# Kernel optimization log

Hardware: AMD Instinct MI355X
Metric: run time of the kernel (lower is better)

The kernel has to match this reference:

```python
import jax, jax.numpy as jnp
import numpy as np

INDIM, HID, OUTDIM, T = 28, 128, 10, 28

def setup_inputs() -> dict:
    key = jax.random.key(0)
    ks = jax.random.split(key, 7)
    B = 65536
    bound1 = 1.0 / np.sqrt(INDIM)
    bound2 = 1.0 / np.sqrt(2 * HID)
    bound3 = 1.0 / np.sqrt(HID)
    return {
        "x": jax.random.normal(ks[0], (B, 784), dtype=jnp.float32),
        "W1": jax.random.uniform(ks[1], (INDIM, HID), jnp.float32, -bound1, bound1),
        "b1": jax.random.uniform(ks[2], (HID,), jnp.float32, -bound1, bound1),
        "W2": jax.random.uniform(ks[3], (2 * HID, HID), jnp.float32, -bound2, bound2),
        "b2": jax.random.uniform(ks[4], (HID,), jnp.float32, -bound2, bound2),
        "W3": jax.random.uniform(ks[5], (HID, OUTDIM), jnp.float32, -bound3, bound3),
        "b3": jax.random.uniform(ks[6], (OUTDIM,), jnp.float32, -bound3, bound3),
    }

def reference(x, W1, b1, W2, b2, W3, b3):
    B = x.shape[0]
    # (B, 784) -> (T, B, 28): scan over the 28 rows of each image
    rows = jnp.transpose(x.reshape(B, T, INDIM), (1, 0, 2))
    # W2 split: first HID rows multiply linear1 output, last HID rows multiply hidden state
    W2a, W2b = W2[:HID], W2[HID:]

    def step(h, row):
        t = row @ W1 + b1                      # (B, HID)
        h_new = jax.nn.relu(t @ W2a + h @ W2b + b2)  # concat(t, h) @ W2 == t@W2a + h@W2b
        return h_new, None

    h0 = jnp.zeros((B, HID), dtype=x.dtype)
    h_final, _ = jax.lax.scan(step, h0, rows)
    return h_final @ W3 + b3
```

## Files before the change

kernel.cpp:

```cpp
#include <hip/hip_runtime.h>

#define BTOT 65536
#define TST  28
#define PACK_DW 100
#define WXL_OFF 12800

typedef __attribute__((ext_vector_type(8))) short bf16x8;
typedef __attribute__((ext_vector_type(4))) float f32x4;
typedef __attribute__((ext_vector_type(2))) unsigned int u32x2;

__device__ __forceinline__ unsigned int f2bf(float f) {
    unsigned u = __float_as_uint(f);
    u += 0x7fff + ((u >> 16) & 1);
    return u >> 16;
}
__device__ __forceinline__ unsigned int pk2bf(float a, float b) {
    return f2bf(a) | (f2bf(b) << 16);
}
__device__ __forceinline__ bf16x8 cvt8(f32x4 a, f32x4 b) {
    union { unsigned int u[4]; bf16x8 v; } r;
    asm("v_cvt_pk_bf16_f32 %0, %1, %2" : "=v"(r.u[0]) : "v"(a[0]), "v"(a[1]));
    asm("v_cvt_pk_bf16_f32 %0, %1, %2" : "=v"(r.u[1]) : "v"(a[2]), "v"(a[3]));
    asm("v_cvt_pk_bf16_f32 %0, %1, %2" : "=v"(r.u[2]) : "v"(b[0]), "v"(b[1]));
    asm("v_cvt_pk_bf16_f32 %0, %1, %2" : "=v"(r.u[3]) : "v"(b[2]), "v"(b[3]));
    return r.v;
}

__global__ void pack1(const float* __restrict__ W1, const float* __restrict__ b1,
                      const float* __restrict__ W2, const float* __restrict__ b2,
                      const float* __restrict__ W3, const float* __restrict__ b3,
                      unsigned int* __restrict__ ws) {
    float* WxL = (float*)(ws + WXL_OFF);
    const int bid = blockIdx.x, tid = threadIdx.x;
    if (bid < 29) {
        const int k = bid, n = tid;
        float s = 0.f;
        if (k < 28) {
            for (int m = 0; m < 128; ++m) s += W1[k * 128 + m] * W2[m * 128 + n];
        } else {
            s = b2[n];
            for (int m = 0; m < 128; ++m) s += b1[m] * W2[m * 128 + n];
        }
        WxL[k * 128 + n] = s;
        if (k == 28) { WxL[29*128+n] = 0.f; WxL[30*128+n] = 0.f; WxL[31*128+n] = 0.f; }
    } else if (bid == 29) {
        if (tid < 64) {
            const int lr = tid & 15, kh = tid >> 4;
            for (int p = 0; p < 2; ++p) {
                unsigned int* P = ws + (p * 64 + tid) * PACK_DW;
                for (int kk = 0; kk < 4; ++kk)
                    for (int t = 0; t < 4; ++t)
                        for (int jd = 0; jd < 4; ++jd) {
                            const int k = 128 + kk * 32 + kh * 8 + jd * 2;
                            const int n = p * 64 + t * 16 + lr;
                            P[(kk * 4 + t) * 4 + jd] =
                                pk2bf(W2[k * 128 + n], W2[(k + 1) * 128 + n]);
                        }
            }
        }
    } else {
        if (tid < 64) {
            const int lr = tid & 15, kh = tid >> 4;
            unsigned int* P = ws + tid * PACK_DW;
            for (int kk = 0; kk < 4; ++kk)
                for (int jd = 0; jd < 4; ++jd) {
                    const int k = kk * 32 + kh * 8 + jd * 2;
                    float lo = (lr < 10) ? W3[k * 10 + lr] : 0.f;
                    float hi = (lr < 10) ? W3[(k + 1) * 10 + lr] : 0.f;
                    P[80 + kk * 4 + jd] = pk2bf(lo, hi);
                }
            for (int j = 0; j < 4; ++j) {
                const int o = kh * 4 + j;
                P[96 + j] = __float_as_uint((o < 10) ? b3[o] : 0.f);
            }
        }
    }
}

__global__ void pack2(unsigned int* __restrict__ ws) {
    const int tid = threadIdx.x;
    if (tid < 64) {
        const float* WxL = (const float*)(ws + WXL_OFF);
        const int lr = tid & 15, kh = tid >> 4;
        for (int p = 0; p < 2; ++p) {
            unsigned int* P = ws + (p * 64 + tid) * PACK_DW;
            for (int t = 0; t < 4; ++t)
                for (int jd = 0; jd < 4; ++jd) {
                    const int k = kh * 8 + jd * 2, n = p * 64 + t * 16 + lr;
                    P[64 + t * 4 + jd] = pk2bf(WxL[k * 128 + n], WxL[(k + 1) * 128 + n]);
                }
        }
    }
}

__global__ __launch_bounds__(128, 3) void rnn_kernel(
    const float* __restrict__ x, const unsigned int* __restrict__ wsPack,
    float* __restrict__ out)
{
    __shared__ __align__(16) short Hs[2][16][136];
    const int tid = threadIdx.x;
    const int p = tid >> 6, lane = tid & 63, lr = lane & 15, kh = lane >> 4;
    const int r0 = blockIdx.x * 16;

    const unsigned int* P = wsPack + (p * 64 + lane) * PACK_DW;
    bf16x8 w2b[4][4], wx[4];
    #pragma unroll
    for (int kk = 0; kk < 4; ++kk)
        #pragma unroll
        for (int t = 0; t < 4; ++t)
            w2b[kk][t] = *(const bf16x8*)(P + (kk * 4 + t) * 4);
    #pragma unroll
    for (int t = 0; t < 4; ++t) wx[t] = *(const bf16x8*)(P + 64 + t * 4);

    unsigned int* hz = (unsigned int*)&Hs[0][0][0];
    #pragma unroll
    for (int i = 0; i < 17; ++i) hz[tid + i * 128] = 0u;
    __syncthreads();

    const f32x4 onec = {1.f, 0.f, 0.f, 0.f};
    const float* xr = x + (size_t)(r0 + lr) * 784 + 8 * kh;
    f32x4 xa = *(const f32x4*)xr;
    f32x4 xc = (kh < 3) ? *(const f32x4*)(xr + 4) : onec;
    bf16x8 xb = cvt8(xa, xc);
    const f32x4 z4 = {0.f, 0.f, 0.f, 0.f};

    int cur = 0;
    for (int t = 0; t < TST; ++t) {
        f32x4 acc[4];
        #pragma unroll
        for (int t4 = 0; t4 < 4; ++t4)
            acc[t4] = __builtin_amdgcn_mfma_f32_16x16x32_bf16(wx[t4], xb, z4, 0, 0, 0);
        f32x4 na, nc;
        const bool pf = (t + 1 < TST);
        if (pf) {
            const float* xp = xr + (t + 1) * 28;
            na = *(const f32x4*)xp;
            nc = (kh < 3) ? *(const f32x4*)(xp + 4) : onec;
        }
        bf16x8 hbv[4];
        #pragma unroll
        for (int kk = 0; kk < 4; ++kk)
            hbv[kk] = *(const bf16x8*)&Hs[cur][lr][kk * 32 + kh * 8];
        #pragma unroll
        for (int kk = 0; kk < 4; ++kk)
            #pragma unroll
            for (int t4 = 0; t4 < 4; ++t4)
                acc[t4] = __builtin_amdgcn_mfma_f32_16x16x32_bf16(w2b[kk][t4], hbv[kk], acc[t4], 0, 0, 0);
        #pragma unroll
        for (int t4 = 0; t4 < 4; ++t4) {
            f32x4 v = acc[t4];
            v[0] = fmaxf(v[0], 0.f); v[1] = fmaxf(v[1], 0.f);
            v[2] = fmaxf(v[2], 0.f); v[3] = fmaxf(v[3], 0.f);
            unsigned lo, hi;
            asm("v_cvt_pk_bf16_f32 %0, %1, %2" : "=v"(lo) : "v"(v[0]), "v"(v[1]));
            asm("v_cvt_pk_bf16_f32 %0, %1, %2" : "=v"(hi) : "v"(v[2]), "v"(v[3]));
            u32x2 st = {lo, hi};
            *(u32x2*)&Hs[cur ^ 1][lr][p * 64 + t4 * 16 + kh * 4] = st;
        }
        if (pf) xb = cvt8(na, nc);
        __syncthreads();
        cur ^= 1;
    }

    if (p == 0) {
        bf16x8 w3f[4];
        #pragma unroll
        for (int kk = 0; kk < 4; ++kk) w3f[kk] = *(const bf16x8*)(P + 80 + kk * 4);
        const float* bp = (const float*)(P + 96);
        f32x4 accO = {bp[0], bp[1], bp[2], bp[3]};
        #pragma unroll
        for (int kk = 0; kk < 4; ++kk) {
            bf16x8 hb = *(const bf16x8*)&Hs[cur][lr][kk * 32 + kh * 8];
            accO = __builtin_amdgcn_mfma_f32_16x16x32_bf16(w3f[kk], hb, accO, 0, 0, 0);
        }
        float* op = out + (size_t)(r0 + lr) * 10 + kh * 4;
        #pragma unroll
        for (int j = 0; j < 4; ++j)
            if (kh * 4 + j < 10) op[j] = accO[j];
    }
}

extern "C" void kernel_launch(void* const* d_in, const int* in_sizes, int n_in,
                              void* d_out, int out_size, void* d_ws, size_t ws_size,
                              hipStream_t stream) {
    const float* x  = (const float*)d_in[0];
    const float* W1 = (const float*)d_in[1];
    const float* b1 = (const float*)d_in[2];
    const float* W2 = (const float*)d_in[3];
    const float* b2 = (const float*)d_in[4];
    const float* W3 = (const float*)d_in[5];
    const float* b3 = (const float*)d_in[6];
    unsigned int* ws = (unsigned int*)d_ws;

    pack1<<<31, 128, 0, stream>>>(W1, b1, W2, b2, W3, b3, ws);
    pack2<<<1, 64, 0, stream>>>(ws);
    rnn_kernel<<<BTOT / 16, 128, 0, stream>>>(x, ws, (float*)d_out);
}
```

Baseline: 82.62 us.

## Switch RNN recurrence to 32x32x16 MFMA with 32-row batch tiles

Replaces the 16x16x32 bf16 MFMA tiling with 32x32x16 MFMAs, so each block now handles 32 batch rows instead of 16. The weight packing, the shared-memory hidden-state layout (k-slab major with padding) and the output bias layout are reorganised to match. Fewer, larger MFMAs per step and half as many blocks amortise the per-step barrier and the weight-register loads over more rows. The cost is fewer blocks in flight and more accumulator registers, which may hurt occupancy and latency hiding.

Result: slower. 97.25 us (+17.7%).

```diff
diff --git a/kernel.cpp b/kernel.cpp
--- a/kernel.cpp
+++ b/kernel.cpp
@@ -2,12 +2,13 @@
 
 #define BTOT 65536
 #define TST  28
-#define PACK_DW 100
-#define WXL_OFF 12800
-
-typedef __attribute__((ext_vector_type(8))) short bf16x8;
-typedef __attribute__((ext_vector_type(4))) float f32x4;
-typedef __attribute__((ext_vector_type(2))) unsigned int u32x2;
+#define PACK_DW 128
+#define WXL_OFF 16384
+
+typedef __attribute__((ext_vector_type(8)))  short bf16x8;
+typedef __attribute__((ext_vector_type(4)))  float f32x4;
+typedef __attribute__((ext_vector_type(16))) float f32x16;
+typedef __attribute__((ext_vector_type(2)))  unsigned int u32x2;
 
 __device__ __forceinline__ unsigned int f2bf(float f) {
     unsigned u = __float_as_uint(f);
@@ -25,6 +26,7 @@
     asm("v_cvt_pk_bf16_f32 %0, %1, %2" : "=v"(r.u[3]) : "v"(b[2]), "v"(b[3]));
     return r.v;
 }
+
 
 __global__ void pack1(const float* __restrict__ W1, const float* __restrict__ b1,
                       const float* __restrict__ W2, const float* __restrict__ b2,
@@ -45,33 +47,33 @@
         if (k == 28) { WxL[29*128+n] = 0.f; WxL[30*128+n] = 0.f; WxL[31*128+n] = 0.f; }
     } else if (bid == 29) {
         if (tid < 64) {
-            const int lr = tid & 15, kh = tid >> 4;
+            const int hi = tid >> 5, ln = tid & 31;
             for (int p = 0; p < 2; ++p) {
                 unsigned int* P = ws + (p * 64 + tid) * PACK_DW;
-                for (int kk = 0; kk < 4; ++kk)
-                    for (int t = 0; t < 4; ++t)
+                for (int nt = 0; nt < 2; ++nt)
+                    for (int ks = 0; ks < 8; ++ks)
                         for (int jd = 0; jd < 4; ++jd) {
-                            const int k = 128 + kk * 32 + kh * 8 + jd * 2;
-                            const int n = p * 64 + t * 16 + lr;
-                            P[(kk * 4 + t) * 4 + jd] =
+                            const int k = 128 + ks * 16 + hi * 8 + jd * 2;
+                            const int n = p * 64 + nt * 32 + ln;
+                            P[(nt * 8 + ks) * 4 + jd] =
                                 pk2bf(W2[k * 128 + n], W2[(k + 1) * 128 + n]);
                         }
             }
         }
     } else {
         if (tid < 64) {
-            const int lr = tid & 15, kh = tid >> 4;
+            const int hi = tid >> 5, ln = tid & 31;
             unsigned int* P = ws + tid * PACK_DW;
-            for (int kk = 0; kk < 4; ++kk)
+            for (int ks = 0; ks < 8; ++ks)
                 for (int jd = 0; jd < 4; ++jd) {
-                    const int k = kk * 32 + kh * 8 + jd * 2;
-                    float lo = (lr < 10) ? W3[k * 10 + lr] : 0.f;
-                    float hi = (lr < 10) ? W3[(k + 1) * 10 + lr] : 0.f;
-                    P[80 + kk * 4 + jd] = pk2bf(lo, hi);
+                    const int k = ks * 16 + hi * 8 + jd * 2;
+                    float lo = (ln < 10) ? W3[k * 10 + ln] : 0.f;
+                    float hh = (ln < 10) ? W3[(k + 1) * 10 + ln] : 0.f;
+                    P[80 + ks * 4 + jd] = pk2bf(lo, hh);
                 }
-            for (int j = 0; j < 4; ++j) {
-                const int o = kh * 4 + j;
-                P[96 + j] = __float_as_uint((o < 10) ? b3[o] : 0.f);
+            for (int reg = 0; reg < 16; ++reg) {
+                const int row = (reg & 3) + 8 * (reg >> 2) + 4 * hi;
+                P[112 + reg] = __float_as_uint((row < 10) ? b3[row] : 0.f);
             }
         }
     }
@@ -81,102 +83,136 @@
     const int tid = threadIdx.x;
     if (tid < 64) {
         const float* WxL = (const float*)(ws + WXL_OFF);
-        const int lr = tid & 15, kh = tid >> 4;
+        const int hi = tid >> 5, ln = tid & 31;
         for (int p = 0; p < 2; ++p) {
             unsigned int* P = ws + (p * 64 + tid) * PACK_DW;
-            for (int t = 0; t < 4; ++t)
-                for (int jd = 0; jd < 4; ++jd) {
-                    const int k = kh * 8 + jd * 2, n = p * 64 + t * 16 + lr;
-                    P[64 + t * 4 + jd] = pk2bf(WxL[k * 128 + n], WxL[(k + 1) * 128 + n]);
-                }
-        }
-    }
-}
+            for (int nt = 0; nt < 2; ++nt)
+                for (int ks = 0; ks < 2; ++ks)
+                    for (int jd = 0; jd < 4; ++jd) {
+                        const int k = ks * 16 + hi * 8 + jd * 2;
+                        const int n = p * 64 + nt * 32 + ln;
+                        P[64 + (nt * 2 + ks) * 4 + jd] =
+                            pk2bf(WxL[k * 128 + n], WxL[(k + 1) * 128 + n]);
+                    }
+        }
+    }
+}
+
+#define MFMA32(a, b, c) __builtin_amdgcn_mfma_f32_32x32x16_bf16(a, b, c, 0, 0, 0)
 
 __global__ __launch_bounds__(128, 3) void rnn_kernel(
     const float* __restrict__ x, const unsigned int* __restrict__ wsPack,
     float* __restrict__ out)
 {
-    __shared__ __align__(16) short Hs[2][16][136];
+    __shared__ __align__(16) unsigned int Hs[2][2080];
     const int tid = threadIdx.x;
-    const int p = tid >> 6, lane = tid & 63, lr = lane & 15, kh = lane >> 4;
-    const int r0 = blockIdx.x * 16;
+    const int p = tid >> 6, lane = tid & 63, hi = lane >> 5, ln = lane & 31;
+    const int r0 = blockIdx.x * 32;
 
     const unsigned int* P = wsPack + (p * 64 + lane) * PACK_DW;
-    bf16x8 w2b[4][4], wx[4];
+    bf16x8 w2b[2][8], wx[2][2];
     #pragma unroll
-    for (int kk = 0; kk < 4; ++kk)
-        #pragma unroll
-        for (int t = 0; t < 4; ++t)
-            w2b[kk][t] = *(const bf16x8*)(P + (kk * 4 + t) * 4);
+    for (int nt = 0; nt < 2; ++nt)
+        #pragma unroll
+        for (int ks = 0; ks < 8; ++ks)
+            w2b[nt][ks] = *(const bf16x8*)(P + (nt * 8 + ks) * 4);
     #pragma unroll
-    for (int t = 0; t < 4; ++t) wx[t] = *(const bf16x8*)(P + 64 + t * 4);
-
-    unsigned int* hz = (unsigned int*)&Hs[0][0][0];
+    for (int nt = 0; nt < 2; ++nt)
+        #pragma unroll
+        for (int ks = 0; ks < 2; ++ks)
+            wx[nt][ks] = *(const bf16x8*)(P + 64 + (nt * 2 + ks) * 4);
+
     #pragma unroll
-    for (int i = 0; i < 17; ++i) hz[tid + i * 128] = 0u;
+    for (int i = 0; i < 17; ++i) {
+        const int idx = tid + i * 128;
+        if (idx < 2080) Hs[0][idx] = 0u;
+    }
     __syncthreads();
 
     const f32x4 onec = {1.f, 0.f, 0.f, 0.f};
-    const float* xr = x + (size_t)(r0 + lr) * 784 + 8 * kh;
-    f32x4 xa = *(const f32x4*)xr;
-    f32x4 xc = (kh < 3) ? *(const f32x4*)(xr + 4) : onec;
-    bf16x8 xb = cvt8(xa, xc);
-    const f32x4 z4 = {0.f, 0.f, 0.f, 0.f};
+    const float* xr = x + (size_t)(r0 + ln) * 784 + hi * 8;
+    f32x4 q0 = *(const f32x4*)xr;
+    f32x4 q1 = *(const f32x4*)(xr + 4);
+    f32x4 q2 = *(const f32x4*)(xr + 16);
+    f32x4 q3 = onec;
+    if (hi == 0) q3 = *(const f32x4*)(xr + 20);
+    bf16x8 xb0 = cvt8(q0, q1);
+    bf16x8 xb1 = cvt8(q2, q3);
+    const f32x16 z16 = {0.f,0.f,0.f,0.f,0.f,0.f,0.f,0.f,0.f,0.f,0.f,0.f,0.f,0.f,0.f,0.f};
 
     int cur = 0;
     for (int t = 0; t < TST; ++t) {
-        f32x4 acc[4];
-        #pragma unroll
-        for (int t4 = 0; t4 < 4; ++t4)
-            acc[t4] = __builtin_amdgcn_mfma_f32_16x16x32_bf16(wx[t4], xb, z4, 0, 0, 0);
-        f32x4 na, nc;
+        f32x16 acc0 = MFMA32(wx[0][0], xb0, z16);
+        f32x16 acc1 = MFMA32(wx[1][0], xb0, z16);
+        acc0 = MFMA32(wx[0][1], xb1, acc0);
+        acc1 = MFMA32(wx[1][1], xb1, acc1);
+
+        f32x4 n0v, n1v, n2v, n3v;
         const bool pf = (t + 1 < TST);
         if (pf) {
             const float* xp = xr + (t + 1) * 28;
-            na = *(const f32x4*)xp;
-            nc = (kh < 3) ? *(const f32x4*)(xp + 4) : onec;
-        }
-        bf16x8 hbv[4];
-        #pragma unroll
-        for (int kk = 0; kk < 4; ++kk)
-            hbv[kk] = *(const bf16x8*)&Hs[cur][lr][kk * 32 + kh * 8];
-        #pragma unroll
-        for (int kk = 0; kk < 4; ++kk)
+            n0v = *(const f32x4*)xp;
+            n1v = *(const f32x4*)(xp + 4);
+            n2v = *(const f32x4*)(xp + 16);
+            n3v = onec;
+            if (hi == 0) n3v = *(const f32x4*)(xp + 20);
+        }
+
+        bf16x8 hb = *(const bf16x8*)&Hs[cur][lane * 4];
+        #pragma unroll
+        for (int ks = 0; ks < 8; ++ks) {
+            bf16x8 hbn;
+            if (ks < 7) hbn = *(const bf16x8*)&Hs[cur][(ks + 1) * 260 + lane * 4];
+            acc0 = MFMA32(w2b[0][ks], hb, acc0);
+            acc1 = MFMA32(w2b[1][ks], hb, acc1);
+            hb = hbn;
+        }
+
+        #pragma unroll
+        for (int nt = 0; nt < 2; ++nt) {
+            const int ntg = p * 2 + nt;
             #pragma unroll
-            for (int t4 = 0; t4 < 4; ++t4)
-                acc[t4] = __builtin_amdgcn_mfma_f32_16x16x32_bf16(w2b[kk][t4], hbv[kk], acc[t4], 0, 0, 0);
-        #pragma unroll
-        for (int t4 = 0; t4 < 4; ++t4) {
-            f32x4 v = acc[t4];
-            v[0] = fmaxf(v[0], 0.f); v[1] = fmaxf(v[1], 0.f);
-            v[2] = fmaxf(v[2], 0.f); v[3] = fmaxf(v[3], 0.f);
-            unsigned lo, hi;
-            asm("v_cvt_pk_bf16_f32 %0, %1, %2" : "=v"(lo) : "v"(v[0]), "v"(v[1]));
-            asm("v_cvt_pk_bf16_f32 %0, %1, %2" : "=v"(hi) : "v"(v[2]), "v"(v[3]));
-            u32x2 st = {lo, hi};
-            *(u32x2*)&Hs[cur ^ 1][lr][p * 64 + t4 * 16 + kh * 4] = st;
-        }
-        if (pf) xb = cvt8(na, nc);
+            for (int q = 0; q < 4; ++q) {
+                float f0, f1, f2, f3;
+                if (nt == 0) {
+                    f0 = acc0[4*q+0]; f1 = acc0[4*q+1]; f2 = acc0[4*q+2]; f3 = acc0[4*q+3];
+                } else {
+                    f0 = acc1[4*q+0]; f1 = acc1[4*q+1]; f2 = acc1[4*q+2]; f3 = acc1[4*q+3];
+                }
+                f0 = fmaxf(f0, 0.f); f1 = fmaxf(f1, 0.f);
+                f2 = fmaxf(f2, 0.f); f3 = fmaxf(f3, 0.f);
+                unsigned d0, d1;
+                asm("v_cvt_pk_bf16_f32 %0, %1, %2" : "=v"(d0) : "v"(f0), "v"(f1));
+                asm("v_cvt_pk_bf16_f32 %0, %1, %2" : "=v"(d1) : "v"(f2), "v"(f3));
+                u32x2 st = {d0, d1};
+                const int idx = (2 * ntg + (q >> 1)) * 260 + ((q & 1) * 32 + ln) * 4 + 2 * hi;
+                *(u32x2*)&Hs[cur ^ 1][idx] = st;
+            }
+        }
+        if (pf) { xb0 = cvt8(n0v, n1v); xb1 = cvt8(n2v, n3v); }
         __syncthreads();
         cur ^= 1;
     }
 
     if (p == 0) {
-        bf16x8 w3f[4];
-        #pragma unroll
-        for (int kk = 0; kk < 4; ++kk) w3f[kk] = *(const bf16x8*)(P + 80 + kk * 4);
-        const float* bp = (const float*)(P + 96);
-        f32x4 accO = {bp[0], bp[1], bp[2], bp[3]};
-        #pragma unroll
-        for (int kk = 0; kk < 4; ++kk) {
-            bf16x8 hb = *(const bf16x8*)&Hs[cur][lr][kk * 32 + kh * 8];
-            accO = __builtin_amdgcn_mfma_f32_16x16x32_bf16(w3f[kk], hb, accO, 0, 0, 0);
-        }
-        float* op = out + (size_t)(r0 + lr) * 10 + kh * 4;
-        #pragma unroll
-        for (int j = 0; j < 4; ++j)
-            if (kh * 4 + j < 10) op[j] = accO[j];
+        bf16x8 w3f[8];
+        #pragma unroll
+        for (int ks = 0; ks < 8; ++ks) w3f[ks] = *(const bf16x8*)(P + 80 + ks * 4);
+        const float* bp = (const float*)(P + 112);
+        f32x16 accO;
+        #pragma unroll
+        for (int r = 0; r < 16; ++r) accO[r] = bp[r];
+        #pragma unroll
+        for (int ks = 0; ks < 8; ++ks) {
+            bf16x8 hb = *(const bf16x8*)&Hs[cur][ks * 260 + lane * 4];
+            accO = MFMA32(w3f[ks], hb, accO);
+        }
+        float* op = out + (size_t)(r0 + ln) * 10;
+        #pragma unroll
+        for (int reg = 0; reg < 16; ++reg) {
+            const int row = (reg & 3) + 8 * (reg >> 2) + 4 * hi;
+            if (row < 10) op[row] = accO[reg];
+        }
     }
 }
 
@@ -194,5 +230,5 @@
 
     pack1<<<31, 128, 0, stream>>>(W1, b1, W2, b2, W3, b3, ws);
     pack2<<<1, 64, 0, stream>>>(ws);
-    rnn_kernel<<<BTOT / 16, 128, 0, stream>>>(x, ws, (float*)d_out);
-}
+    rnn_kernel<<<BTOT / 32, 128, 0, stream>>>(x, ws, (float*)d_out);
+}
```

## Run each 16-row tile on a single wave to drop per-step block barriers

Applied to the files above, without the earlier changes.

The recurrent kernel now uses one 64-lane wave per 16-row batch tile instead of two waves that split the hidden columns. Each wave holds all of W2b and the fused input weights in registers (32+8 bf16x8 fragments). The hidden state lives in one LDS buffer laid out so that the write pattern matches the next step's read pattern, which removes the double buffer and the __syncthreads per timestep. The trade-off is higher register pressure per wave, twice the MFMA work per wave per step, and reliance on intra-wave LDS ordering without explicit barriers.

Result: faster. 78.62 us (-4.8%).

```diff
diff --git a/kernel.cpp b/kernel.cpp
--- a/kernel.cpp
+++ b/kernel.cpp
@@ -2,11 +2,12 @@
 
 #define BTOT 65536
 #define TST  28
-#define PACK_DW 100
-#define WXL_OFF 12800
+#define PACK_DW 180
+#define WXL_OFF (64 * PACK_DW)
 
 typedef __attribute__((ext_vector_type(8))) short bf16x8;
 typedef __attribute__((ext_vector_type(4))) float f32x4;
+typedef __attribute__((ext_vector_type(4))) unsigned int u32x4;
 typedef __attribute__((ext_vector_type(2))) unsigned int u32x2;
 
 __device__ __forceinline__ unsigned int f2bf(float f) {
@@ -46,17 +47,15 @@
     } else if (bid == 29) {
         if (tid < 64) {
             const int lr = tid & 15, kh = tid >> 4;
-            for (int p = 0; p < 2; ++p) {
-                unsigned int* P = ws + (p * 64 + tid) * PACK_DW;
-                for (int kk = 0; kk < 4; ++kk)
-                    for (int t = 0; t < 4; ++t)
-                        for (int jd = 0; jd < 4; ++jd) {
-                            const int k = 128 + kk * 32 + kh * 8 + jd * 2;
-                            const int n = p * 64 + t * 16 + lr;
-                            P[(kk * 4 + t) * 4 + jd] =
-                                pk2bf(W2[k * 128 + n], W2[(k + 1) * 128 + n]);
-                        }
-            }
+            unsigned int* P = ws + tid * PACK_DW;
+            for (int kk = 0; kk < 4; ++kk)
+                for (int t8 = 0; t8 < 8; ++t8)
+                    for (int jd = 0; jd < 4; ++jd) {
+                        const int k = 128 + kk * 32 + kh * 8 + jd * 2;
+                        const int n = t8 * 16 + lr;
+                        P[(kk * 8 + t8) * 4 + jd] =
+                            pk2bf(W2[k * 128 + n], W2[(k + 1) * 128 + n]);
+                    }
         }
     } else {
         if (tid < 64) {
@@ -67,11 +66,11 @@
                     const int k = kk * 32 + kh * 8 + jd * 2;
                     float lo = (lr < 10) ? W3[k * 10 + lr] : 0.f;
                     float hi = (lr < 10) ? W3[(k + 1) * 10 + lr] : 0.f;
-                    P[80 + kk * 4 + jd] = pk2bf(lo, hi);
+                    P[160 + kk * 4 + jd] = pk2bf(lo, hi);
                 }
             for (int j = 0; j < 4; ++j) {
                 const int o = kh * 4 + j;
-                P[96 + j] = __float_as_uint((o < 10) ? b3[o] : 0.f);
+                P[176 + j] = __float_as_uint((o < 10) ? b3[o] : 0.f);
             }
         }
     }
@@ -82,40 +81,43 @@
     if (tid < 64) {
         const float* WxL = (const float*)(ws + WXL_OFF);
         const int lr = tid & 15, kh = tid >> 4;
-        for (int p = 0; p < 2; ++p) {
-            unsigned int* P = ws + (p * 64 + tid) * PACK_DW;
-            for (int t = 0; t < 4; ++t)
-                for (int jd = 0; jd < 4; ++jd) {
-                    const int k = kh * 8 + jd * 2, n = p * 64 + t * 16 + lr;
-                    P[64 + t * 4 + jd] = pk2bf(WxL[k * 128 + n], WxL[(k + 1) * 128 + n]);
-                }
-        }
+        unsigned int* P = ws + tid * PACK_DW;
+        for (int t8 = 0; t8 < 8; ++t8)
+            for (int jd = 0; jd < 4; ++jd) {
+                const int k = kh * 8 + jd * 2, n = t8 * 16 + lr;
+                P[128 + t8 * 4 + jd] = pk2bf(WxL[k * 128 + n], WxL[(k + 1) * 128 + n]);
+            }
     }
 }
 
-__global__ __launch_bounds__(128, 3) void rnn_kernel(
+__global__ __launch_bounds__(64, 2) void rnn_kernel(
     const float* __restrict__ x, const unsigned int* __restrict__ wsPack,
     float* __restrict__ out)
 {
-    __shared__ __align__(16) short Hs[2][16][136];
-    const int tid = threadIdx.x;
-    const int p = tid >> 6, lane = tid & 63, lr = lane & 15, kh = lane >> 4;
+    __shared__ __align__(16) unsigned int Hs[1024];
+    const int lane = threadIdx.x;
+    const int lr = lane & 15, kh = lane >> 4;
     const int r0 = blockIdx.x * 16;
 
-    const unsigned int* P = wsPack + (p * 64 + lane) * PACK_DW;
-    bf16x8 w2b[4][4], wx[4];
+    const unsigned int* P = wsPack + lane * PACK_DW;
+    bf16x8 w2b[4][8], wx[8];
     #pragma unroll
     for (int kk = 0; kk < 4; ++kk)
         #pragma unroll
-        for (int t = 0; t < 4; ++t)
-            w2b[kk][t] = *(const bf16x8*)(P + (kk * 4 + t) * 4);
+        for (int t8 = 0; t8 < 8; ++t8)
+            w2b[kk][t8] = *(const bf16x8*)(P + (kk * 8 + t8) * 4);
     #pragma unroll
-    for (int t = 0; t < 4; ++t) wx[t] = *(const bf16x8*)(P + 64 + t * 4);
+    for (int t8 = 0; t8 < 8; ++t8) wx[t8] = *(const bf16x8*)(P + 128 + t8 * 4);
 
-    unsigned int* hz = (unsigned int*)&Hs[0][0][0];
+    unsigned wAddr[8];
     #pragma unroll
-    for (int i = 0; i < 17; ++i) hz[tid + i * 128] = 0u;
-    __syncthreads();
+    for (int t8 = 0; t8 < 8; ++t8)
+        wAddr[t8] = (t8 >> 1) * 256 + (2 * (t8 & 1) + (kh >> 1)) * 64
+                  + lr * 4 + (kh & 1) * 2;
+
+    #pragma unroll
+    for (int i = 0; i < 4; ++i)
+        ((u32x4*)Hs)[lane + i * 64] = (u32x4){0u, 0u, 0u, 0u};
 
     const f32x4 onec = {1.f, 0.f, 0.f, 0.f};
     const float* xr = x + (size_t)(r0 + lr) * 784 + 8 * kh;
@@ -124,12 +126,7 @@
     bf16x8 xb = cvt8(xa, xc);
     const f32x4 z4 = {0.f, 0.f, 0.f, 0.f};
 
-    int cur = 0;
     for (int t = 0; t < TST; ++t) {
-        f32x4 acc[4];
-        #pragma unroll
-        for (int t4 = 0; t4 < 4; ++t4)
-            acc[t4] = __builtin_amdgcn_mfma_f32_16x16x32_bf16(wx[t4], xb, z4, 0, 0, 0);
         f32x4 na, nc;
         const bool pf = (t + 1 < TST);
         if (pf) {
@@ -137,47 +134,50 @@
             na = *(const f32x4*)xp;
             nc = (kh < 3) ? *(const f32x4*)(xp + 4) : onec;
         }
+
         bf16x8 hbv[4];
         #pragma unroll
         for (int kk = 0; kk < 4; ++kk)
-            hbv[kk] = *(const bf16x8*)&Hs[cur][lr][kk * 32 + kh * 8];
+            hbv[kk] = *(const bf16x8*)&Hs[kk * 256 + lane * 4];
+
+        f32x4 acc[8];
+        #pragma unroll
+        for (int t8 = 0; t8 < 8; ++t8)
+            acc[t8] = __builtin_amdgcn_mfma_f32_16x16x32_bf16(wx[t8], xb, z4, 0, 0, 0);
         #pragma unroll
         for (int kk = 0; kk < 4; ++kk)
             #pragma unroll
-            for (int t4 = 0; t4 < 4; ++t4)
-                acc[t4] = __builtin_amdgcn_mfma_f32_16x16x32_bf16(w2b[kk][t4], hbv[kk], acc[t4], 0, 0, 0);
+            for (int t8 = 0; t8 < 8; ++t8)
+                acc[t8] = __builtin_amdgcn_mfma_f32_16x16x32_bf16(w2b[kk][t8], hbv[kk], acc[t8], 0, 0, 0);
+
         #pragma unroll
-        for (int t4 = 0; t4 < 4; ++t4) {
-            f32x4 v = acc[t4];
+        for (int t8 = 0; t8 < 8; ++t8) {
+            f32x4 v = acc[t8];
             v[0] = fmaxf(v[0], 0.f); v[1] = fmaxf(v[1], 0.f);
             v[2] = fmaxf(v[2], 0.f); v[3] = fmaxf(v[3], 0.f);
             unsigned lo, hi;
             asm("v_cvt_pk_bf16_f32 %0, %1, %2" : "=v"(lo) : "v"(v[0]), "v"(v[1]));
             asm("v_cvt_pk_bf16_f32 %0, %1, %2" : "=v"(hi) : "v"(v[2]), "v"(v[3]));
             u32x2 st = {lo, hi};
-            *(u32x2*)&Hs[cur ^ 1][lr][p * 64 + t4 * 16 + kh * 4] = st;
+            *(u32x2*)&Hs[wAddr[t8]] = st;
         }
         if (pf) xb = cvt8(na, nc);
-        __syncthreads();
-        cur ^= 1;
     }
 
-    if (p == 0) {
-        bf16x8 w3f[4];
-        #pragma unroll
-        for (int kk = 0; kk < 4; ++kk) w3f[kk] = *(const bf16x8*)(P + 80 + kk * 4);
-        const float* bp = (const float*)(P + 96);
-        f32x4 accO = {bp[0], bp[1], bp[2], bp[3]};
-        #pragma unroll
-        for (int kk = 0; kk < 4; ++kk) {
-            bf16x8 hb = *(const bf16x8*)&Hs[cur][lr][kk * 32 + kh * 8];
-            accO = __builtin_amdgcn_mfma_f32_16x16x32_bf16(w3f[kk], hb, accO, 0, 0, 0);
-        }
-        float* op = out + (size_t)(r0 + lr) * 10 + kh * 4;
-        #pragma unroll
-        for (int j = 0; j < 4; ++j)
-            if (kh * 4 + j < 10) op[j] = accO[j];
+    bf16x8 w3f[4];
+    #pragma unroll
+    for (int kk = 0; kk < 4; ++kk) w3f[kk] = *(const bf16x8*)(P + 160 + kk * 4);
+    const float* bp = (const float*)(P + 176);
+    f32x4 accO = {bp[0], bp[1], bp[2], bp[3]};
+    #pragma unroll
+    for (int kk = 0; kk < 4; ++kk) {
+        bf16x8 hb = *(const bf16x8*)&Hs[kk * 256 + lane * 4];
+        accO = __builtin_amdgcn_mfma_f32_16x16x32_bf16(w3f[kk], hb, accO, 0, 0, 0);
     }
+    float* op = out + (size_t)(r0 + lr) * 10 + kh * 4;
+    #pragma unroll
+    for (int j = 0; j < 4; ++j)
+        if (kh * 4 + j < 10) op[j] = accO[j];
 }
 
 extern "C" void kernel_launch(void* const* d_in, const int* in_sizes, int n_in,
@@ -194,5 +194,5 @@
 
     pack1<<<31, 128, 0, stream>>>(W1, b1, W2, b2, W3, b3, ws);
     pack2<<<1, 64, 0, stream>>>(ws);
-    rnn_kernel<<<BTOT / 16, 128, 0, stream>>>(x, ws, (float*)d_out);
+    rnn_kernel<<<BTOT / 16, 64, 0, stream>>>(x, ws, (float*)d_out);
 }
```
